# Kernel tuning notes

Measured on AMD Instinct MI355X. Metric: run time of the kernel, lower is better.

Reference implementation:

```python
import jax, jax.numpy as jnp
import numpy as np

B_, M_, SD, CD, LD, HW = 2048, 64, 32, 8, 128, 512


def setup_inputs() -> dict:
    key = jax.random.key(0)
    ks = jax.random.split(key, 12)
    def n(k, shp, scale=1.0):
        return jax.random.normal(k, shp, dtype=jnp.float32) * scale
    w = 0.05  # small weight init so the M-step linear recurrence stays stable
    return dict(
        x_k=n(ks[0], (B_, SD)),
        u_seq=n(ks[1], (B_, M_, CD)),
        x_next_seq=n(ks[2], (B_, M_, SD)),
        enc_w0=n(ks[3], (SD, HW), w), enc_b0=jnp.zeros((HW,), jnp.float32),
        enc_w1=n(ks[4], (HW, HW), w), enc_b1=jnp.zeros((HW,), jnp.float32),
        enc_w2=n(ks[5], (HW, HW), w), enc_b2=jnp.zeros((HW,), jnp.float32),
        enc_w3=n(ks[6], (HW, LD), w), enc_b3=jnp.zeros((LD,), jnp.float32),
        A_w=n(ks[7], (LD, LD), w),   # z_next = z @ A_w  (no bias)
        B_w=n(ks[8], (CD, LD), w),   # + u @ B_w          (no bias)
        C_w=n(ks[9], (LD, SD), w),   # x = z @ C_w + C_b
        C_b=jnp.zeros((SD,), jnp.float32),
    )


def _encode(x, w0, b0, w1, b1, w2, b2, w3, b3):
    h = jax.nn.relu(x @ w0 + b0)
    h = jax.nn.relu(h @ w1 + b1)
    h = jax.nn.relu(h @ w2 + b2)
    return h @ w3 + b3


def reference(x_k, u_seq, x_next_seq,
              enc_w0, enc_b0, enc_w1, enc_b1, enc_w2, enc_b2, enc_w3, enc_b3,
              A_w, B_w, C_w, C_b):
    B, M, sd = x_next_seq.shape
    # encoder on initial state and on all M target states (shared MLP)
    z_k = _encode(x_k, enc_w0, enc_b0, enc_w1, enc_b1, enc_w2, enc_b2, enc_w3, enc_b3)
    z_target_seq = _encode(
        x_next_seq.reshape(B * M, sd),
        enc_w0, enc_b0, enc_w1, enc_b1, enc_w2, enc_b2, enc_w3, enc_b3,
    ).reshape(B, M, -1)
    # precompute B u_i for all steps, then run the linear recurrence with scan
    Bu = jnp.einsum('bmc,cl->mbl', u_seq, B_w)  # [M, B, LD]
    def step(z, bu):
        z_next = z @ A_w + bu
        return z_next, z_next
    _, z_seq = jax.lax.scan(step, z_k, Bu)       # [M, B, LD]
    z_pred_seq = jnp.swapaxes(z_seq, 0, 1)       # [B, M, LD]
    x_pred_seq = z_pred_seq @ C_w + C_b          # linear decoder
    return (z_pred_seq, x_pred_seq, z_target_seq)
```

## Files before the change

kernel.cpp:

```cpp
#include <hip/hip_runtime.h>

#define B_TOT 2048
#define M_SEQ 64
#define SDIM 32
#define CDIM 8
#define LDIM 128
#define HDIM 512

#define NROWS_NEXT (B_TOT * M_SEQ)
#define NROWS_ALL  (NROWS_NEXT + B_TOT)

typedef short bf16x8 __attribute__((ext_vector_type(8)));
typedef float f32x4  __attribute__((ext_vector_type(4)));
typedef float f32x4v __attribute__((ext_vector_type(4)));

__device__ __forceinline__ unsigned short f2bf(float f) {
    unsigned int u = __builtin_bit_cast(unsigned int, f);
    u = u + 0x7FFFu + ((u >> 16) & 1u);
    return (unsigned short)(u >> 16);
}

__device__ __forceinline__ unsigned int swz(unsigned int byte) {
    return byte ^ (((byte >> 10) & 15u) << 4);
}
__device__ __forceinline__ unsigned int swzf(unsigned int byte) {
    return byte ^ (((byte >> 9) & 15u) << 4);
}

__device__ __forceinline__ void pack_one16(const float* __restrict__ W, short* __restrict__ out,
                                           int e, int N) {
    int j    = e & 7;
    int lane = (e >> 3) & 63;
    int tile = e >> 9;
    int NT   = N >> 4;
    int nt   = tile % NT;
    int kt   = tile / NT;
    int k = kt * 32 + ((lane >> 4) << 3) + j;
    int n = (nt << 4) + (lane & 15);
    out[e] = (short)f2bf(W[(size_t)k * N + n]);
}

#define P_S0 16384
#define P_S1 (P_S0 + 262144)
#define P_S2 (P_S1 + 262144)
#define P_S3 (P_S2 + 65536)

__global__ void pack_all(const float* __restrict__ w0, const float* __restrict__ w1,
                         const float* __restrict__ w2, const float* __restrict__ w3,
                         short* __restrict__ o0, short* __restrict__ o1,
                         short* __restrict__ o2, short* __restrict__ o3) {
    int id = blockIdx.x * 256 + threadIdx.x;
    if (id < P_S0)      pack_one16(w0, o0, id, HDIM);
    else if (id < P_S1) pack_one16(w1, o1, id - P_S0, HDIM);
    else if (id < P_S2) pack_one16(w2, o2, id - P_S1, HDIM);
    else if (id < P_S3) pack_one16(w3, o3, id - P_S2, LDIM);
}

__global__ __launch_bounds__(128) void mm128(const float* __restrict__ X,
                                             const float* __restrict__ Y,
                                             float* __restrict__ O) {
    int r = blockIdx.x, c = threadIdx.x;
    float s = 0.f;
    for (int k = 0; k < 128; ++k) s += X[r * 128 + k] * Y[k * 128 + c];
    O[r * 128 + c] = s;
}

__device__ __forceinline__ void layer_lds(char* hbuf, const short* __restrict__ pw,
                                          const float* __restrict__ bias,
                                          int ktCount, int wave, int lane) {
    const int l15 = lane & 15;
    const int lhi = lane >> 4;
    const unsigned base0 = (unsigned)(l15 * 1024 + (lhi << 4));
    const unsigned xmask = ((unsigned)l15) << 4;

    f32x4 acc[4][4];
    #pragma unroll
    for (int mt = 0; mt < 4; ++mt)
        #pragma unroll
        for (int nt = 0; nt < 4; ++nt)
            acc[mt][nt] = (f32x4){0.f, 0.f, 0.f, 0.f};

    const short* p = pw + (wave << 11) + (lane << 3);
    bf16x8 bcur[4];
    #pragma unroll
    for (int nt = 0; nt < 4; ++nt) bcur[nt] = *(const bf16x8*)(p + (nt << 9));

    for (int kt = 0; kt < ktCount; ++kt) {
        bf16x8 bnext[4];
        if (kt + 1 < ktCount) {
            const short* pn = p + 16384;
            #pragma unroll
            for (int nt = 0; nt < 4; ++nt) bnext[nt] = *(const bf16x8*)(pn + (nt << 9));
        }
        const char* abase = hbuf + ((base0 + (unsigned)kt * 64u) ^ xmask);
        bf16x8 a[4];
        #pragma unroll
        for (int mt = 0; mt < 4; ++mt)
            a[mt] = *(const bf16x8*)(abase + mt * 16384);
        #pragma unroll
        for (int nt = 0; nt < 4; ++nt)
            #pragma unroll
            for (int mt = 0; mt < 4; ++mt)
                acc[mt][nt] = __builtin_amdgcn_mfma_f32_16x16x32_bf16(a[mt], bcur[nt], acc[mt][nt], 0, 0, 0);
        p += 16384;
        if (kt + 1 < ktCount) {
            #pragma unroll
            for (int nt = 0; nt < 4; ++nt) bcur[nt] = bnext[nt];
        }
    }
    __syncthreads();

    #pragma unroll
    for (int nt = 0; nt < 4; ++nt) {
        int colg = (wave * 4 + nt) * 16 + l15;
        float bv = bias[colg];
        #pragma unroll
        for (int mt = 0; mt < 4; ++mt) {
            #pragma unroll
            for (int r = 0; r < 4; ++r) {
                int row = mt * 16 + (lhi << 2) + r;
                float v = fmaxf(acc[mt][nt][r] + bv, 0.f);
                *(unsigned short*)(hbuf + swz((unsigned)(row * 1024 + colg * 2))) = f2bf(v);
            }
        }
    }
    __syncthreads();
}

__global__ __launch_bounds__(512, 4) void encoder_kernel(
    const float* __restrict__ x_next, const float* __restrict__ x_k,
    const short* __restrict__ pw0, const short* __restrict__ pw1,
    const short* __restrict__ pw2, const short* __restrict__ pw3,
    const float* __restrict__ b0, const float* __restrict__ b1,
    const float* __restrict__ b2, const float* __restrict__ b3,
    float* __restrict__ z_target, float* __restrict__ z_k_out) {
    __shared__ __attribute__((aligned(16))) char hbuf[64 * 1024];
    const int tid  = threadIdx.x;
    const int wave = tid >> 6;
    const int lane = tid & 63;
    const int l15  = lane & 15;
    const int lhi  = lane >> 4;
    const int r0   = blockIdx.x * 64;

    const float* xin;
    float* zout;
    bool is_tgt = (r0 < NROWS_NEXT);
    if (is_tgt) {
        xin  = x_next + (size_t)r0 * SDIM;
        zout = z_target + (size_t)r0 * LDIM;
    } else {
        xin  = x_k + (size_t)(r0 - NROWS_NEXT) * SDIM;
        zout = z_k_out + (size_t)(r0 - NROWS_NEXT) * LDIM;
    }

    {
        int row = tid >> 3;
        int c   = (tid & 7) * 4;
        float4 v = *(const float4*)(xin + row * SDIM + c);
        uint2 pk;
        pk.x = (unsigned int)f2bf(v.x) | ((unsigned int)f2bf(v.y) << 16);
        pk.y = (unsigned int)f2bf(v.z) | ((unsigned int)f2bf(v.w) << 16);
        *(uint2*)(hbuf + swz((unsigned)(row * 1024 + c * 2))) = pk;
    }
    __syncthreads();

    layer_lds(hbuf, pw0, b0, 1, wave, lane);
    layer_lds(hbuf, pw1, b1, 16, wave, lane);
    layer_lds(hbuf, pw2, b2, 16, wave, lane);

    {
        const unsigned base0 = (unsigned)(l15 * 1024 + (lhi << 4));
        const unsigned xmask = ((unsigned)l15) << 4;
        f32x4 acc[4];
        #pragma unroll
        for (int mt = 0; mt < 4; ++mt) acc[mt] = (f32x4){0.f, 0.f, 0.f, 0.f};

        const short* p = pw3 + (wave << 9) + (lane << 3);
        bf16x8 bcur = *(const bf16x8*)(p);
        for (int kt = 0; kt < 16; ++kt) {
            bf16x8 bnext;
            if (kt < 15) bnext = *(const bf16x8*)(p + 4096);
            const char* abase = hbuf + ((base0 + (unsigned)kt * 64u) ^ xmask);
            bf16x8 a[4];
            #pragma unroll
            for (int mt = 0; mt < 4; ++mt)
                a[mt] = *(const bf16x8*)(abase + mt * 16384);
            #pragma unroll
            for (int mt = 0; mt < 4; ++mt)
                acc[mt] = __builtin_amdgcn_mfma_f32_16x16x32_bf16(a[mt], bcur, acc[mt], 0, 0, 0);
            p += 4096;
            if (kt < 15) bcur = bnext;
        }
        __syncthreads();

        int colg = wave * 16 + l15;
        float bv = b3[colg];
        #pragma unroll
        for (int mt = 0; mt < 4; ++mt) {
            #pragma unroll
            for (int r = 0; r < 4; ++r) {
                int row = mt * 16 + (lhi << 2) + r;
                *(float*)(hbuf + swzf((unsigned)(row * 512 + colg * 4))) = acc[mt][r] + bv;
            }
        }
        __syncthreads();

        #pragma unroll
        for (int pass = 0; pass < 4; ++pass) {
            unsigned int L = (unsigned)(pass * 512 + tid) * 16;
            f32x4v v = *(const f32x4v*)(hbuf + swzf(L));
            if (is_tgt) __builtin_nontemporal_store(v, (f32x4v*)(zout + (L >> 2)));
            else        *(f32x4v*)(zout + (L >> 2)) = v;
        }
    }
}

#define RR4 4
__global__ __launch_bounds__(512, 4) void recurrence2_kernel(
    const float* __restrict__ zk, const float* __restrict__ u,
    const float* __restrict__ Bw, const float* __restrict__ Aw,
    const float* __restrict__ A2, const float* __restrict__ Cw,
    const float* __restrict__ Cb,
    float* __restrict__ zpred, float* __restrict__ xpred) {
    __shared__ float z_lds[RR4][128];
    __shared__ float part[4][8][128];
    __shared__ float zoutb[2][RR4][128];
    __shared__ float u_lds[RR4 * M_SEQ * CDIM];
    __shared__ float Bw_lds[CDIM * 128];
    __shared__ float Ct_lds[32 * 132];
    __shared__ float cb_lds[SDIM];
    const int tid   = threadIdx.x;
    const int col   = tid & 127;
    const int slice = tid >> 7;
    const int b0    = blockIdx.x * RR4;

    float a1[32], a2r[32], ba[16];
    #pragma unroll
    for (int i = 0; i < 32; ++i) {
        a1[i]  = Aw[(size_t)(slice * 32 + i) * 128 + col];
        a2r[i] = A2[(size_t)(slice * 32 + i) * 128 + col];
    }

    if (tid < RR4 * 128)
        z_lds[tid >> 7][tid & 127] = zk[(size_t)(b0 + (tid >> 7)) * 128 + (tid & 127)];
    for (int id = tid; id < CDIM * 128; id += 512) Bw_lds[id] = Bw[id];
    for (int id = tid; id < RR4 * M_SEQ * CDIM; id += 512)
        u_lds[id] = u[(size_t)b0 * M_SEQ * CDIM + id];
    for (int id = tid; id < 128 * 32; id += 512) {
        int k = id >> 5, c = id & 31;
        Ct_lds[c * 132 + k] = Cw[id];
    }
    if (tid < SDIM) cb_lds[tid] = Cb[tid];
    __syncthreads();

    #pragma unroll
    for (int c = 0; c < 8; ++c) {
        float s = 0.f;
        #pragma unroll
        for (int kk = 0; kk < 32; ++kk) s += Bw_lds[c * 128 + slice * 32 + kk] * a1[kk];
        part[slice][c][col] = s;
    }
    __syncthreads();
    #pragma unroll
    for (int c = 0; c < 8; ++c) {
        ba[c]     = Bw_lds[c * 128 + col];
        ba[8 + c] = part[0][c][col] + part[1][c][col] + part[2][c][col] + part[3][c][col];
    }
    __syncthreads();

    for (int r = 0; r < 32; ++r) {
        const int m0 = 2 * r;
        #pragma unroll
        for (int b = 0; b < RR4; ++b) {
            const float4* z4 = (const float4*)&z_lds[b][slice * 32];
            float p1 = 0.f, p2 = 0.f;
            #pragma unroll
            for (int i = 0; i < 8; ++i) {
                float4 zv = z4[i];
                p1 += a1[i*4+0]*zv.x + a1[i*4+1]*zv.y + a1[i*4+2]*zv.z + a1[i*4+3]*zv.w;
                p2 += a2r[i*4+0]*zv.x + a2r[i*4+1]*zv.y + a2r[i*4+2]*zv.z + a2r[i*4+3]*zv.w;
            }
            part[slice][b * 2 + 0][col] = p1;
            part[slice][b * 2 + 1][col] = p2;
        }
        if (r > 0 && tid < 256) {
            const int mprev = 2 * (r - 1);
            int sb = tid >> 5, c32 = tid & 31;
            int s = sb >> 2, b = sb & 3;
            float acc = cb_lds[c32];
            const float4* z4 = (const float4*)&zoutb[s][b][0];
            const float4* c4 = (const float4*)&Ct_lds[c32 * 132];
            #pragma unroll
            for (int i = 0; i < 32; ++i) {
                float4 zv = z4[i], cv = c4[i];
                acc += zv.x*cv.x + zv.y*cv.y + zv.z*cv.z + zv.w*cv.w;
            }
            __builtin_nontemporal_store(acc,
                xpred + ((size_t)(b0 + b) * M_SEQ + (mprev + s)) * SDIM + c32);
        }
        __syncthreads();
        {
            const int b = slice;
            float v0 = part[0][b*2+0][col] + part[1][b*2+0][col] + part[2][b*2+0][col] + part[3][b*2+0][col];
            float v1 = part[0][b*2+1][col] + part[1][b*2+1][col] + part[2][b*2+1][col] + part[3][b*2+1][col];
            const float4* uu0 = (const float4*)&u_lds[(b * M_SEQ + m0) * CDIM];
            float4 ua = uu0[0], ub = uu0[1];
            v0 += ua.x*ba[0] + ua.y*ba[1] + ua.z*ba[2] + ua.w*ba[3]
                + ub.x*ba[4] + ub.y*ba[5] + ub.z*ba[6] + ub.w*ba[7];
            v1 += ua.x*ba[8] + ua.y*ba[9] + ua.z*ba[10] + ua.w*ba[11]
                + ub.x*ba[12] + ub.y*ba[13] + ub.z*ba[14] + ub.w*ba[15];
            const float4* uu1 = (const float4*)&u_lds[(b * M_SEQ + m0 + 1) * CDIM];
            float4 uc = uu1[0], ud = uu1[1];
            v1 += uc.x*ba[0] + uc.y*ba[1] + uc.z*ba[2] + uc.w*ba[3]
                + ud.x*ba[4] + ud.y*ba[5] + ud.z*ba[6] + ud.w*ba[7];
            zoutb[0][b][col] = v0;
            zoutb[1][b][col] = v1;
            z_lds[b][col] = v1;
            __builtin_nontemporal_store(v0, zpred + ((size_t)(b0 + b) * M_SEQ + m0) * 128 + col);
            __builtin_nontemporal_store(v1, zpred + ((size_t)(b0 + b) * M_SEQ + m0 + 1) * 128 + col);
        }
        __syncthreads();
    }
    if (tid < 256) {
        const int mprev = 62;
        int sb = tid >> 5, c32 = tid & 31;
        int s = sb >> 2, b = sb & 3;
        float acc = cb_lds[c32];
        const float4* z4 = (const float4*)&zoutb[s][b][0];
        const float4* c4 = (const float4*)&Ct_lds[c32 * 132];
        #pragma unroll
        for (int i = 0; i < 32; ++i) {
            float4 zv = z4[i], cv = c4[i];
            acc += zv.x*cv.x + zv.y*cv.y + zv.z*cv.z + zv.w*cv.w;
        }
        __builtin_nontemporal_store(acc,
            xpred + ((size_t)(b0 + b) * M_SEQ + (mprev + s)) * SDIM + c32);
    }
}

extern "C" void kernel_launch(void* const* d_in, const int* in_sizes, int n_in,
                              void* d_out, int out_size, void* d_ws, size_t ws_size,
                              hipStream_t stream) {
    const float* x_k    = (const float*)d_in[0];
    const float* u_seq  = (const float*)d_in[1];
    const float* x_next = (const float*)d_in[2];
    const float* w0 = (const float*)d_in[3];  const float* b0 = (const float*)d_in[4];
    const float* w1 = (const float*)d_in[5];  const float* b1 = (const float*)d_in[6];
    const float* w2 = (const float*)d_in[7];  const float* b2 = (const float*)d_in[8];
    const float* w3 = (const float*)d_in[9];  const float* b3 = (const float*)d_in[10];
    const float* A_w = (const float*)d_in[11];
    const float* B_w = (const float*)d_in[12];
    const float* C_w = (const float*)d_in[13];
    const float* C_b = (const float*)d_in[14];

    float* out    = (float*)d_out;
    float* z_pred = out;
    float* x_pred = out + (size_t)NROWS_NEXT * LDIM;
    float* z_tgt  = x_pred + (size_t)NROWS_NEXT * SDIM;

    char* ws = (char*)d_ws;
    short* pw0 = (short*)(ws);
    short* pw1 = (short*)(ws + 32768);
    short* pw2 = (short*)(ws + 32768 + 524288);
    short* pw3 = (short*)(ws + 32768 + 2 * 524288);
    float* z_k_buf = (float*)(ws + 32768 + 2 * 524288 + 131072);
    float* A2_buf  = (float*)(ws + 32768 + 2 * 524288 + 131072 + 1048576);

    mm128<<<128, 128, 0, stream>>>(A_w, A_w, A2_buf);

    pack_all<<<(P_S3 + 255) / 256, 256, 0, stream>>>(w0, w1, w2, w3, pw0, pw1, pw2, pw3);

    encoder_kernel<<<NROWS_ALL / 64, 512, 0, stream>>>(
        x_next, x_k, pw0, pw1, pw2, pw3, b0, b1, b2, b3, z_tgt, z_k_buf);

    recurrence2_kernel<<<B_TOT / RR4, 512, 0, stream>>>(
        z_k_buf, u_seq, B_w, A_w, A2_buf, C_w, C_b, z_pred, x_pred);
}
```

Baseline: 446.1 us.

## Halve encoder row tile to 32 rows for higher occupancy, drop B prefetch

```diff
diff --git a/kernel.cpp b/kernel.cpp
--- a/kernel.cpp
+++ b/kernel.cpp
@@ -65,48 +65,35 @@
     O[r * 128 + c] = s;
 }
 
-__device__ __forceinline__ void layer_lds(char* hbuf, const short* __restrict__ pw,
-                                          const float* __restrict__ bias,
-                                          int ktCount, int wave, int lane) {
+__device__ __forceinline__ void layer32r(char* hbuf, const short* __restrict__ pw,
+                                         const float* __restrict__ bias,
+                                         int ktCount, int wave, int lane) {
     const int l15 = lane & 15;
     const int lhi = lane >> 4;
     const unsigned base0 = (unsigned)(l15 * 1024 + (lhi << 4));
     const unsigned xmask = ((unsigned)l15) << 4;
 
-    f32x4 acc[4][4];
-    #pragma unroll
-    for (int mt = 0; mt < 4; ++mt)
+    f32x4 acc[2][4];
+    #pragma unroll
+    for (int mt = 0; mt < 2; ++mt)
         #pragma unroll
         for (int nt = 0; nt < 4; ++nt)
             acc[mt][nt] = (f32x4){0.f, 0.f, 0.f, 0.f};
 
     const short* p = pw + (wave << 11) + (lane << 3);
-    bf16x8 bcur[4];
-    #pragma unroll
-    for (int nt = 0; nt < 4; ++nt) bcur[nt] = *(const bf16x8*)(p + (nt << 9));
-
     for (int kt = 0; kt < ktCount; ++kt) {
-        bf16x8 bnext[4];
-        if (kt + 1 < ktCount) {
-            const short* pn = p + 16384;
-            #pragma unroll
-            for (int nt = 0; nt < 4; ++nt) bnext[nt] = *(const bf16x8*)(pn + (nt << 9));
-        }
-        const char* abase = hbuf + ((base0 + (unsigned)kt * 64u) ^ xmask);
-        bf16x8 a[4];
-        #pragma unroll
-        for (int mt = 0; mt < 4; ++mt)
-            a[mt] = *(const bf16x8*)(abase + mt * 16384);
-        #pragma unroll
-        for (int nt = 0; nt < 4; ++nt)
-            #pragma unroll
-            for (int mt = 0; mt < 4; ++mt)
-                acc[mt][nt] = __builtin_amdgcn_mfma_f32_16x16x32_bf16(a[mt], bcur[nt], acc[mt][nt], 0, 0, 0);
+        bf16x8 b[4];
+        #pragma unroll
+        for (int nt = 0; nt < 4; ++nt) b[nt] = *(const bf16x8*)(p + (nt << 9));
+        const char* ab = hbuf + ((base0 + (unsigned)kt * 64u) ^ xmask);
+        bf16x8 a0 = *(const bf16x8*)(ab);
+        bf16x8 a1 = *(const bf16x8*)(ab + 16384);
+        #pragma unroll
+        for (int nt = 0; nt < 4; ++nt) {
+            acc[0][nt] = __builtin_amdgcn_mfma_f32_16x16x32_bf16(a0, b[nt], acc[0][nt], 0, 0, 0);
+            acc[1][nt] = __builtin_amdgcn_mfma_f32_16x16x32_bf16(a1, b[nt], acc[1][nt], 0, 0, 0);
+        }
         p += 16384;
-        if (kt + 1 < ktCount) {
-            #pragma unroll
-            for (int nt = 0; nt < 4; ++nt) bcur[nt] = bnext[nt];
-        }
     }
     __syncthreads();
 
@@ -115,7 +102,7 @@
         int colg = (wave * 4 + nt) * 16 + l15;
         float bv = bias[colg];
         #pragma unroll
-        for (int mt = 0; mt < 4; ++mt) {
+        for (int mt = 0; mt < 2; ++mt) {
             #pragma unroll
             for (int r = 0; r < 4; ++r) {
                 int row = mt * 16 + (lhi << 2) + r;
@@ -127,20 +114,20 @@
     __syncthreads();
 }
 
-__global__ __launch_bounds__(512, 4) void encoder_kernel(
+__global__ __launch_bounds__(512, 6) void encoder_kernel(
     const float* __restrict__ x_next, const float* __restrict__ x_k,
     const short* __restrict__ pw0, const short* __restrict__ pw1,
     const short* __restrict__ pw2, const short* __restrict__ pw3,
     const float* __restrict__ b0, const float* __restrict__ b1,
     const float* __restrict__ b2, const float* __restrict__ b3,
     float* __restrict__ z_target, float* __restrict__ z_k_out) {
-    __shared__ __attribute__((aligned(16))) char hbuf[64 * 1024];
+    __shared__ __attribute__((aligned(16))) char hbuf[32 * 1024];
     const int tid  = threadIdx.x;
     const int wave = tid >> 6;
     const int lane = tid & 63;
     const int l15  = lane & 15;
     const int lhi  = lane >> 4;
-    const int r0   = blockIdx.x * 64;
+    const int r0   = blockIdx.x * 32;
 
     const float* xin;
     float* zout;
@@ -153,7 +140,7 @@
         zout = z_k_out + (size_t)(r0 - NROWS_NEXT) * LDIM;
     }
 
-    {
+    if (tid < 256) {
         int row = tid >> 3;
         int c   = (tid & 7) * 4;
         float4 v = *(const float4*)(xin + row * SDIM + c);
@@ -164,39 +151,33 @@
     }
     __syncthreads();
 
-    layer_lds(hbuf, pw0, b0, 1, wave, lane);
-    layer_lds(hbuf, pw1, b1, 16, wave, lane);
-    layer_lds(hbuf, pw2, b2, 16, wave, lane);
+    layer32r(hbuf, pw0, b0, 1, wave, lane);
+    layer32r(hbuf, pw1, b1, 16, wave, lane);
+    layer32r(hbuf, pw2, b2, 16, wave, lane);
 
     {
         const unsigned base0 = (unsigned)(l15 * 1024 + (lhi << 4));
         const unsigned xmask = ((unsigned)l15) << 4;
-        f32x4 acc[4];
-        #pragma unroll
-        for (int mt = 0; mt < 4; ++mt) acc[mt] = (f32x4){0.f, 0.f, 0.f, 0.f};
+        f32x4 acc[2];
+        acc[0] = (f32x4){0.f, 0.f, 0.f, 0.f};
+        acc[1] = (f32x4){0.f, 0.f, 0.f, 0.f};
 
         const short* p = pw3 + (wave << 9) + (lane << 3);
-        bf16x8 bcur = *(const bf16x8*)(p);
         for (int kt = 0; kt < 16; ++kt) {
-            bf16x8 bnext;
-            if (kt < 15) bnext = *(const bf16x8*)(p + 4096);
-            const char* abase = hbuf + ((base0 + (unsigned)kt * 64u) ^ xmask);
-            bf16x8 a[4];
-            #pragma unroll
-            for (int mt = 0; mt < 4; ++mt)
-                a[mt] = *(const bf16x8*)(abase + mt * 16384);
-            #pragma unroll
-            for (int mt = 0; mt < 4; ++mt)
-                acc[mt] = __builtin_amdgcn_mfma_f32_16x16x32_bf16(a[mt], bcur, acc[mt], 0, 0, 0);
+            bf16x8 b = *(const bf16x8*)(p);
+            const char* ab = hbuf + ((base0 + (unsigned)kt * 64u) ^ xmask);
+            bf16x8 a0 = *(const bf16x8*)(ab);
+            bf16x8 a1 = *(const bf16x8*)(ab + 16384);
+            acc[0] = __builtin_amdgcn_mfma_f32_16x16x32_bf16(a0, b, acc[0], 0, 0, 0);
+            acc[1] = __builtin_amdgcn_mfma_f32_16x16x32_bf16(a1, b, acc[1], 0, 0, 0);
             p += 4096;
-            if (kt < 15) bcur = bnext;
         }
         __syncthreads();
 
         int colg = wave * 16 + l15;
         float bv = b3[colg];
         #pragma unroll
-        for (int mt = 0; mt < 4; ++mt) {
+        for (int mt = 0; mt < 2; ++mt) {
             #pragma unroll
             for (int r = 0; r < 4; ++r) {
                 int row = mt * 16 + (lhi << 2) + r;
@@ -206,7 +187,7 @@
         __syncthreads();
 
         #pragma unroll
-        for (int pass = 0; pass < 4; ++pass) {
+        for (int pass = 0; pass < 2; ++pass) {
             unsigned int L = (unsigned)(pass * 512 + tid) * 16;
             f32x4v v = *(const f32x4v*)(hbuf + swzf(L));
             if (is_tgt) __builtin_nontemporal_store(v, (f32x4v*)(zout + (L >> 2)));
@@ -370,7 +351,7 @@
 
     pack_all<<<(P_S3 + 255) / 256, 256, 0, stream>>>(w0, w1, w2, w3, pw0, pw1, pw2, pw3);
 
-    encoder_kernel<<<NROWS_ALL / 64, 512, 0, stream>>>(
+    encoder_kernel<<<NROWS_ALL / 32, 512, 0, stream>>>(
         x_next, x_k, pw0, pw1, pw2, pw3, b0, b1, b2, b3, z_tgt, z_k_buf);
 
     recurrence2_kernel<<<B_TOT / RR4, 512, 0, stream>>>(
```

New measurement: 494.5 us. +10.9%, slower.
